# Performance work log

Measured on AMD Instinct MI355X. Metric: run time of the kernel, lower is better.

## Reference

```python
import jax, jax.numpy as jnp
import numpy as np

N = 10000
E = 160000
DIMS = [512, 512, 512, 256]  # in -> hidden -> hidden -> out (num_layers=3)
EPS = 1e-12  # F.normalize default eps


def _sage_layer(x, edge_index, Wl, b, Wr):
    # PyG SAGEConv (mean aggr, normalize=True):
    # out = lin_l(mean_{j in N(i)} x_j) + lin_r(x_i), then L2-normalize rows.
    src = edge_index[0]
    dst = edge_index[1]
    msg = x[src]  # [E, d] gather of source-node features
    agg = jax.ops.segment_sum(msg, dst, num_segments=N)  # [N, d]
    cnt = jax.ops.segment_sum(jnp.ones((E,), x.dtype), dst, num_segments=N)
    mean = agg / jnp.maximum(cnt, 1.0)[:, None]
    out = mean @ Wl.T + b + x @ Wr.T
    norm = jnp.sqrt(jnp.sum(out * out, axis=-1, keepdims=True))
    return out / jnp.maximum(norm, EPS)


def setup_inputs() -> dict:
    key = jax.random.key(0)
    ks = jax.random.split(key, 2 + 3 * len(DIMS))
    x = jax.random.normal(ks[0], (N, DIMS[0]), dtype=jnp.float32)
    edge_index = jax.random.randint(ks[1], (2, E), 0, N, dtype=jnp.int64)
    inp = {"x": x, "edge_index": edge_index}
    k = 2
    for i in range(len(DIMS) - 1):
        din, dout = DIMS[i], DIMS[i + 1]
        s = 1.0 / np.sqrt(din)
        inp[f"Wl{i}"] = jax.random.uniform(ks[k], (dout, din), jnp.float32, -s, s); k += 1
        inp[f"b{i}"] = jax.random.uniform(ks[k], (dout,), jnp.float32, -s, s); k += 1
        inp[f"Wr{i}"] = jax.random.uniform(ks[k], (dout, din), jnp.float32, -s, s); k += 1
    return inp


def reference(x, edge_index, Wl0, b0, Wr0, Wl1, b1, Wr1, Wl2, b2, Wr2):
    params = [(Wl0, b0, Wr0), (Wl1, b1, Wr1), (Wl2, b2, Wr2)]
    for Wl, b, Wr in params:
        x = _sage_layer(x, edge_index, Wl, b, Wr)
        x = jax.nn.relu(x)
        # F.dropout(training=False) is identity at inference
    return x
```

## Files before the change

kernel.cpp:

```cpp
#include <hip/hip_runtime.h>

#define NN 10000

typedef __attribute__((ext_vector_type(8))) short short8;
typedef __attribute__((ext_vector_type(4))) float f32x4;
typedef __attribute__((ext_vector_type(8))) _Float16 h16x8;
typedef __attribute__((ext_vector_type(4))) _Float16 h16x4;

__device__ __forceinline__ ushort f2b(float f) {
    union { float f; uint32_t u; } v; v.f = f;
    uint32_t u = v.u;
    return (ushort)((u + 0x7fffu + ((u >> 16) & 1u)) >> 16);
}
__device__ __forceinline__ uint packbf(float a, float b) {
    return (uint)f2b(a) | ((uint)f2b(b) << 16);
}
__device__ __forceinline__ float blo(uint u) {
    union { uint u; float f; } v; v.u = u << 16; return v.f;
}
__device__ __forceinline__ float bhi(uint u) {
    union { uint u; float f; } v; v.u = u & 0xffff0000u; return v.f;
}

__global__ __launch_bounds__(256) void count_dst(const int* __restrict__ dst,
                                                 int* __restrict__ counts, int E) {
    int i = blockIdx.x * 256 + threadIdx.x;
    if (i < E) atomicAdd(&counts[dst[i]], 1);
}

__global__ __launch_bounds__(256) void scan_local(const int* __restrict__ counts,
                                                  int* __restrict__ lpref,
                                                  int* __restrict__ bsum, int n) {
    __shared__ int tmp[256];
    int t = threadIdx.x, b = blockIdx.x;
    int i = b * 256 + t;
    int c = (i < n) ? counts[i] : 0;
    tmp[t] = c;
    __syncthreads();
    for (int off = 1; off < 256; off <<= 1) {
        int v = (t >= off) ? tmp[t - off] : 0;
        __syncthreads();
        tmp[t] += v;
        __syncthreads();
    }
    if (i < n) lpref[i] = tmp[t] - c;
    if (t == 255) bsum[b] = tmp[255];
}

__global__ __launch_bounds__(256) void scan_apply(const int* __restrict__ counts,
                                                  const int* __restrict__ lpref,
                                                  const int* __restrict__ bsum,
                                                  int* __restrict__ offsets,
                                                  int* __restrict__ cursor,
                                                  float* __restrict__ inv_cnt, int n) {
    __shared__ int sbase;
    int t = threadIdx.x, b = blockIdx.x;
    if (t == 0) {
        int s = 0;
        for (int j = 0; j < b; j++) s += bsum[j];
        sbase = s;
    }
    __syncthreads();
    int i = b * 256 + t;
    if (i < n) {
        int c = counts[i];
        int o = sbase + lpref[i];
        offsets[i] = o;
        cursor[i]  = o;
        inv_cnt[i] = 1.0f / fmaxf((float)c, 1.0f);
    }
}

__global__ __launch_bounds__(256) void scatter_edges(const int* __restrict__ src,
                                                     const int* __restrict__ dst,
                                                     int* __restrict__ cursor,
                                                     int* __restrict__ sorted_src, int E) {
    int i = blockIdx.x * 256 + threadIdx.x;
    if (i < E) {
        int p = atomicAdd(&cursor[dst[i]], 1);
        sorted_src[p] = src[i];
    }
}

__global__ __launch_bounds__(256) void cvt_all(const float* __restrict__ x,
                                               const float* __restrict__ Wl0,
                                               const float* __restrict__ Wr0,
                                               const float* __restrict__ Wl1,
                                               const float* __restrict__ Wr1,
                                               const float* __restrict__ Wl2,
                                               const float* __restrict__ Wr2,
                                               ushort* __restrict__ xbuf,
                                               ushort* __restrict__ Wc0,
                                               ushort* __restrict__ Wc1,
                                               ushort* __restrict__ Wc2,
                                               int* __restrict__ counts) {
    int i = blockIdx.x * 256 + threadIdx.x;
    const float* src;
    ushort* dst;
    if (i < 1280000) {
        int idx = i * 4;
        src = x + idx;
        dst = xbuf + idx;
    } else if (i < 1411072) {
        int j = (i - 1280000) * 4;
        int row = j >> 9, col = j & 511;
        src = (row < 512) ? (Wl0 + (size_t)row * 512 + col)
                          : (Wr0 + (size_t)(row - 512) * 512 + col);
        dst = Wc0 + j;
    } else if (i < 1542144) {
        int j = (i - 1411072) * 4;
        int row = j >> 9, col = j & 511;
        src = (row < 512) ? (Wl1 + (size_t)row * 512 + col)
                          : (Wr1 + (size_t)(row - 512) * 512 + col);
        dst = Wc1 + j;
    } else if (i < 1607680) {
        int j = (i - 1542144) * 4;
        int row = j >> 9, col = j & 511;
        src = (row < 256) ? (Wl2 + (size_t)row * 512 + col)
                          : (Wr2 + (size_t)(row - 256) * 512 + col);
        dst = Wc2 + j;
    } else if (i < 1610180) {
        int t = i - 1607680;
        int4 z = {0, 0, 0, 0};
        *(int4*)(counts + t * 4) = z;
        return;
    } else {
        return;
    }
    float4 v = *(const float4*)src;
    uint2 p;
    p.x = packbf(v.x, v.y);
    p.y = packbf(v.z, v.w);
    *(uint2*)dst = p;
}

__global__ __launch_bounds__(256) void gemm_split(const ushort* __restrict__ A,
                                                  const ushort* __restrict__ B,
                                                  ushort* __restrict__ G,
                                                  _Float16* __restrict__ R,
                                                  int M, int dout) {
    __shared__ ushort Asl[2][128 * 32];
    __shared__ ushort Bsl[2][128 * 32];
    const int tid  = threadIdx.x;
    const int w    = tid >> 6;
    const int lane = tid & 63;

    const int nbx = gridDim.x, nby = gridDim.y;
    const int nwg = nbx * nby;
    const int id  = blockIdx.y * nbx + blockIdx.x;
    const int qq  = nwg >> 3, rr = nwg & 7;
    const int xcd = id & 7, blk = id >> 3;
    const int swzid = (xcd < rr ? xcd * (qq + 1) : rr * (qq + 1) + (xcd - rr) * qq) + blk;
    const int bx = swzid % nbx, by = swzid / nbx;

    const int bm = by * 128, bn = bx * 128;
    const int wm = (w & 1) * 64, wn = (w >> 1) * 64;
    const int row16 = lane & 15, q = lane >> 4;

    f32x4 acc[4][4];
#pragma unroll
    for (int i = 0; i < 4; i++)
#pragma unroll
        for (int j = 0; j < 4; j++) acc[i][j] = (f32x4){0.f, 0.f, 0.f, 0.f};

    const int sc_r = lane >> 2;
    const int sc_s = lane & 3;
    const int koff = sc_s ^ ((sc_r >> 1) & 3);
    const int swz  = (row16 >> 1) & 3;

    auto stage = [&](int buf, int k0) {
#pragma unroll
        for (int c = 0; c < 2; c++) {
            int chunk = w * 2 + c;
            int rloc  = chunk * 16 + sc_r;
            int growA = bm + rloc; growA = growA < M ? growA : M - 1;
            const ushort* gpA = A + (size_t)growA * 512 + k0 + koff * 8;
            __builtin_amdgcn_global_load_lds(
                (const __attribute__((address_space(1))) uint32_t*)gpA,
                (__attribute__((address_space(3))) uint32_t*)&Asl[buf][chunk * 512],
                16, 0, 0);
            const ushort* gpB = B + (size_t)(bn + rloc) * 512 + k0 + koff * 8;
            __builtin_amdgcn_global_load_lds(
                (const __attribute__((address_space(1))) uint32_t*)gpB,
                (__attribute__((address_space(3))) uint32_t*)&Bsl[buf][chunk * 512],
                16, 0, 0);
        }
    };

    const int NT = 512 / 32;
    stage(0, 0);
    asm volatile("s_waitcnt vmcnt(0)" ::: "memory");
    __builtin_amdgcn_sched_barrier(0);
    __builtin_amdgcn_s_barrier();
    int cur = 0;

    for (int t = 0; t < NT; ++t) {
        const bool pref = (t + 1 < NT);
        if (pref) {
            stage(cur ^ 1, (t + 1) * 32);
            asm volatile("s_waitcnt vmcnt(4)" ::: "memory");
        } else {
            asm volatile("s_waitcnt vmcnt(0)" ::: "memory");
        }
        __builtin_amdgcn_sched_barrier(0);
        __builtin_amdgcn_s_barrier();

        short8 af[4], bfr[4];
        int s = q ^ swz;
#pragma unroll
        for (int i = 0; i < 4; i++) {
            int r = wm + i * 16 + row16;
            af[i] = *(const short8*)&Asl[cur][r * 32 + s * 8];
        }
#pragma unroll
        for (int j = 0; j < 4; j++) {
            int rn = wn + j * 16 + row16;
            bfr[j] = *(const short8*)&Bsl[cur][rn * 32 + s * 8];
        }
#pragma unroll
        for (int i = 0; i < 4; i++)
#pragma unroll
            for (int j = 0; j < 4; j++)
                acc[i][j] = __builtin_amdgcn_mfma_f32_16x16x32_bf16(
                    af[i], bfr[j], acc[i][j], 0, 0, 0);

        __builtin_amdgcn_sched_barrier(0);
        __builtin_amdgcn_s_barrier();
        cur ^= 1;
    }

    const bool isR = (bn >= dout);
#pragma unroll
    for (int i = 0; i < 4; i++) {
#pragma unroll
        for (int r2 = 0; r2 < 4; r2++) {
            int row = bm + wm + i * 16 + q * 4 + r2;
            if (row < M) {
                if (isR) {
                    _Float16* Rp = R + (size_t)row * dout + (bn - dout) + wn + row16;
#pragma unroll
                    for (int j = 0; j < 4; j++)
                        Rp[j * 16] = (_Float16)acc[i][j][r2];
                } else {
                    ushort* Gp = G + (size_t)row * dout + bn + wn + row16;
#pragma unroll
                    for (int j = 0; j < 4; j++)
                        Gp[j * 16] = f2b(acc[i][j][r2]);
                }
            }
        }
    }
}

template <int DOUT, bool FINAL>
__global__ __launch_bounds__(256) void aggfin(const ushort* __restrict__ G,
                                              const _Float16* __restrict__ R,
                                              const float* __restrict__ bias,
                                              const int* __restrict__ offsets,
                                              const int* __restrict__ counts,
                                              const int* __restrict__ sorted_src,
                                              const float* __restrict__ inv_cnt,
                                              ushort* __restrict__ xnext,
                                              float* __restrict__ outf, int n) {
    constexpr int PL = DOUT / 64;
    int wave = threadIdx.x >> 6;
    int lane = threadIdx.x & 63;
    int node = blockIdx.x * 4 + wave;
    if (node >= n) return;
    int start = offsets[node];
    int cnt   = counts[node];
    float inv = inv_cnt[node];

    float acc[PL];
#pragma unroll
    for (int k = 0; k < PL; k++) acc[k] = 0.f;

    if constexpr (DOUT == 512) {
        const uint* gp = (const uint*)G + lane * 4;
#define ACC8(v) do { \
        acc[0] += blo(v.x); acc[1] += bhi(v.x); \
        acc[2] += blo(v.y); acc[3] += bhi(v.y); \
        acc[4] += blo(v.z); acc[5] += bhi(v.z); \
        acc[6] += blo(v.w); acc[7] += bhi(v.w); } while (0)
        int e = 0;
        for (; e + 8 <= cnt; e += 8) {
            uint4 vv[8];
#pragma unroll
            for (int u = 0; u < 8; u++) {
                int s0 = sorted_src[start + e + u];
                vv[u] = *(const uint4*)(gp + (size_t)s0 * 256);
            }
#pragma unroll
            for (int u = 0; u < 8; u++) ACC8(vv[u]);
        }
        for (; e < cnt; e++) {
            int s0 = sorted_src[start + e];
            uint4 v0 = *(const uint4*)(gp + (size_t)s0 * 256);
            ACC8(v0);
        }
#undef ACC8
    } else {
        const uint* gp = (const uint*)G + lane * 2;
#define ACC4(v) do { \
        acc[0] += blo(v.x); acc[1] += bhi(v.x); \
        acc[2] += blo(v.y); acc[3] += bhi(v.y); } while (0)
        int e = 0;
        for (; e + 8 <= cnt; e += 8) {
            uint2 vv[8];
#pragma unroll
            for (int u = 0; u < 8; u++) {
                int s0 = sorted_src[start + e + u];
                vv[u] = *(const uint2*)(gp + (size_t)s0 * 128);
            }
#pragma unroll
            for (int u = 0; u < 8; u++) ACC4(vv[u]);
        }
        for (; e < cnt; e++) {
            int s0 = sorted_src[start + e];
            uint2 v0 = *(const uint2*)(gp + (size_t)s0 * 128);
            ACC4(v0);
        }
#undef ACC4
    }

    float v[PL];
    const _Float16* Rp = R + (size_t)node * DOUT + lane * PL;
    const float* Bp = bias + lane * PL;
    if constexpr (PL == 8) {
        h16x8 hv = *(const h16x8*)Rp;
#pragma unroll
        for (int k = 0; k < PL; k += 4) {
            float4 b4 = *(const float4*)(Bp + k);
            v[k + 0] = acc[k + 0] * inv + (float)hv[k + 0] + b4.x;
            v[k + 1] = acc[k + 1] * inv + (float)hv[k + 1] + b4.y;
            v[k + 2] = acc[k + 2] * inv + (float)hv[k + 2] + b4.z;
            v[k + 3] = acc[k + 3] * inv + (float)hv[k + 3] + b4.w;
        }
    } else {
        h16x4 hv = *(const h16x4*)Rp;
#pragma unroll
        for (int k = 0; k < PL; k += 4) {
            float4 b4 = *(const float4*)(Bp + k);
            v[k + 0] = acc[k + 0] * inv + (float)hv[k + 0] + b4.x;
            v[k + 1] = acc[k + 1] * inv + (float)hv[k + 1] + b4.y;
            v[k + 2] = acc[k + 2] * inv + (float)hv[k + 2] + b4.z;
            v[k + 3] = acc[k + 3] * inv + (float)hv[k + 3] + b4.w;
        }
    }

    float ss = 0.f;
#pragma unroll
    for (int k = 0; k < PL; k++) ss += v[k] * v[k];
#pragma unroll
    for (int m = 32; m >= 1; m >>= 1) ss += __shfl_xor(ss, m, 64);
    float scale = 1.0f / fmaxf(sqrtf(ss), 1e-12f);

    if constexpr (FINAL) {
        float* Op = outf + (size_t)node * DOUT + lane * PL;
#pragma unroll
        for (int k = 0; k < PL; k += 4) {
            float4 o;
            o.x = fmaxf(v[k + 0] * scale, 0.f);
            o.y = fmaxf(v[k + 1] * scale, 0.f);
            o.z = fmaxf(v[k + 2] * scale, 0.f);
            o.w = fmaxf(v[k + 3] * scale, 0.f);
            *(float4*)(Op + k) = o;
        }
    } else {
        uint4 o;
        float r0 = fmaxf(v[0] * scale, 0.f), r1 = fmaxf(v[1] * scale, 0.f);
        float r2 = fmaxf(v[2] * scale, 0.f), r3 = fmaxf(v[3] * scale, 0.f);
        float r4 = fmaxf(v[4] * scale, 0.f), r5 = fmaxf(v[5] * scale, 0.f);
        float r6 = fmaxf(v[6] * scale, 0.f), r7 = fmaxf(v[7] * scale, 0.f);
        o.x = packbf(r0, r1); o.y = packbf(r2, r3);
        o.z = packbf(r4, r5); o.w = packbf(r6, r7);
        *(uint4*)(xnext + (size_t)node * 512 + lane * 8) = o;
    }
}

extern "C" void kernel_launch(void* const* d_in, const int* in_sizes, int n_in,
                              void* d_out, int out_size, void* d_ws, size_t ws_size,
                              hipStream_t stream) {
    const float* x    = (const float*)d_in[0];
    const int*   edge = (const int*)d_in[1];
    const float* Wl0  = (const float*)d_in[2];
    const float* b0   = (const float*)d_in[3];
    const float* Wr0  = (const float*)d_in[4];
    const float* Wl1  = (const float*)d_in[5];
    const float* b1   = (const float*)d_in[6];
    const float* Wr1  = (const float*)d_in[7];
    const float* Wl2  = (const float*)d_in[8];
    const float* b2   = (const float*)d_in[9];
    const float* Wr2  = (const float*)d_in[10];

    const int E = in_sizes[1] / 2;

    char* ws = (char*)d_ws;
    int*      counts  = (int*)(ws + 0);
    int*      offsets = (int*)(ws + 40960);
    int*      cursor  = (int*)(ws + 81920);
    float*    invc    = (float*)(ws + 122880);
    int*      sorted  = (int*)(ws + 163840);
    ushort*   Wc0     = (ushort*)(ws + 819200);
    ushort*   Wc1     = (ushort*)(ws + 1867776);
    ushort*   Wc2     = (ushort*)(ws + 2916352);
    ushort*   xbuf    = (ushort*)(ws + 3440640);
    ushort*   Gbuf    = (ushort*)(ws + 13680640);
    _Float16* Rbuf    = (_Float16*)(ws + 23920640);
    int*      lpref   = (int*)(ws + 34160640);
    int*      bsum    = (int*)(ws + 34201600);

    cvt_all<<<(1610180 + 255) / 256, 256, 0, stream>>>(x, Wl0, Wr0, Wl1, Wr1, Wl2, Wr2,
                                                       xbuf, Wc0, Wc1, Wc2, counts);

    const int nsb = (NN + 255) / 256;
    count_dst<<<(E + 255) / 256, 256, 0, stream>>>(edge + E, counts, E);
    scan_local<<<nsb, 256, 0, stream>>>(counts, lpref, bsum, NN);
    scan_apply<<<nsb, 256, 0, stream>>>(counts, lpref, bsum, offsets, cursor, invc, NN);
    scatter_edges<<<(E + 255) / 256, 256, 0, stream>>>(edge, edge + E, cursor, sorted, E);

    const int gyM = (NN + 127) / 128;
    const int gb  = (NN + 3) / 4;

    gemm_split<<<dim3(8, gyM), 256, 0, stream>>>(xbuf, Wc0, Gbuf, Rbuf, NN, 512);
    aggfin<512, false><<<gb, 256, 0, stream>>>(Gbuf, Rbuf, b0, offsets, counts,
                                               sorted, invc, xbuf, nullptr, NN);
    gemm_split<<<dim3(8, gyM), 256, 0, stream>>>(xbuf, Wc1, Gbuf, Rbuf, NN, 512);
    aggfin<512, false><<<gb, 256, 0, stream>>>(Gbuf, Rbuf, b1, offsets, counts,
                                               sorted, invc, xbuf, nullptr, NN);
    gemm_split<<<dim3(4, gyM), 256, 0, stream>>>(xbuf, Wc2, Gbuf, Rbuf, NN, 256);
    aggfin<256, true><<<gb, 256, 0, stream>>>(Gbuf, Rbuf, b2, offsets, counts,
                                              sorted, invc, nullptr, (float*)d_out, NN);
}
```

Measured before the change: 233.9 us.

## Bucket CSR edges by source range to improve gather locality

The CSR build now counts edges per (destination, source-bucket) pair, using 16 buckets of 625 nodes each. It scans the 160k-entry count array and scatters edges so that each node's neighbor list is grouped by source range. The aim is more locality in the feature gathers inside aggfin, and a parallel reduction replaces the serial block-sum prefix in scan_apply. The cost is a larger scan (625 blocks instead of 40), an extra atomic per edge and more workspace. The hardcoded 625 divisor assumes N=10000.

```diff
diff --git a/kernel.cpp b/kernel.cpp
--- a/kernel.cpp
+++ b/kernel.cpp
@@ -1,6 +1,7 @@
 #include <hip/hip_runtime.h>
 
 #define NN 10000
+#define NBK 16
 
 typedef __attribute__((ext_vector_type(8))) short short8;
 typedef __attribute__((ext_vector_type(4))) float f32x4;
@@ -22,19 +23,25 @@
     union { uint u; float f; } v; v.u = u & 0xffff0000u; return v.f;
 }
 
-__global__ __launch_bounds__(256) void count_dst(const int* __restrict__ dst,
-                                                 int* __restrict__ counts, int E) {
+__global__ __launch_bounds__(256) void count_dst(const int* __restrict__ src,
+                                                 const int* __restrict__ dst,
+                                                 int* __restrict__ counts,
+                                                 int* __restrict__ counts2, int E) {
     int i = blockIdx.x * 256 + threadIdx.x;
-    if (i < E) atomicAdd(&counts[dst[i]], 1);
-}
-
-__global__ __launch_bounds__(256) void scan_local(const int* __restrict__ counts,
+    if (i < E) {
+        int d = dst[i], s = src[i];
+        atomicAdd(&counts[d], 1);
+        atomicAdd(&counts2[d * NBK + s / 625], 1);
+    }
+}
+
+__global__ __launch_bounds__(256) void scan_local(const int* __restrict__ counts2,
                                                   int* __restrict__ lpref,
                                                   int* __restrict__ bsum, int n) {
     __shared__ int tmp[256];
     int t = threadIdx.x, b = blockIdx.x;
     int i = b * 256 + t;
-    int c = (i < n) ? counts[i] : 0;
+    int c = (i < n) ? counts2[i] : 0;
     tmp[t] = c;
     __syncthreads();
     for (int off = 1; off < 256; off <<= 1) {
@@ -47,38 +54,44 @@
     if (t == 255) bsum[b] = tmp[255];
 }
 
-__global__ __launch_bounds__(256) void scan_apply(const int* __restrict__ counts,
-                                                  const int* __restrict__ lpref,
+__global__ __launch_bounds__(256) void scan_apply(const int* __restrict__ lpref,
                                                   const int* __restrict__ bsum,
-                                                  int* __restrict__ offsets,
-                                                  int* __restrict__ cursor,
+                                                  const int* __restrict__ counts,
+                                                  int* __restrict__ offsets2,
+                                                  int* __restrict__ cursor2,
                                                   float* __restrict__ inv_cnt, int n) {
-    __shared__ int sbase;
+    __shared__ int red[256];
     int t = threadIdx.x, b = blockIdx.x;
-    if (t == 0) {
-        int s = 0;
-        for (int j = 0; j < b; j++) s += bsum[j];
-        sbase = s;
-    }
+    int s = 0;
+    for (int j = t; j < b; j += 256) s += bsum[j];
+    red[t] = s;
     __syncthreads();
+    for (int off = 128; off >= 1; off >>= 1) {
+        if (t < off) red[t] += red[t + off];
+        __syncthreads();
+    }
+    int base = red[0];
     int i = b * 256 + t;
     if (i < n) {
-        int c = counts[i];
-        int o = sbase + lpref[i];
-        offsets[i] = o;
-        cursor[i]  = o;
-        inv_cnt[i] = 1.0f / fmaxf((float)c, 1.0f);
+        int o = base + lpref[i];
+        offsets2[i] = o;
+        cursor2[i]  = o;
+        if ((i & (NBK - 1)) == 0) {
+            int node = i / NBK;
+            inv_cnt[node] = 1.0f / fmaxf((float)counts[node], 1.0f);
+        }
     }
 }
 
 __global__ __launch_bounds__(256) void scatter_edges(const int* __restrict__ src,
                                                      const int* __restrict__ dst,
-                                                     int* __restrict__ cursor,
+                                                     int* __restrict__ cursor2,
                                                      int* __restrict__ sorted_src, int E) {
     int i = blockIdx.x * 256 + threadIdx.x;
     if (i < E) {
-        int p = atomicAdd(&cursor[dst[i]], 1);
-        sorted_src[p] = src[i];
+        int s = src[i], d = dst[i];
+        int p = atomicAdd(&cursor2[d * NBK + s / 625], 1);
+        sorted_src[p] = s;
     }
 }
 
@@ -93,7 +106,8 @@
                                                ushort* __restrict__ Wc0,
                                                ushort* __restrict__ Wc1,
                                                ushort* __restrict__ Wc2,
-                                               int* __restrict__ counts) {
+                                               int* __restrict__ counts,
+                                               int* __restrict__ counts2) {
     int i = blockIdx.x * 256 + threadIdx.x;
     const float* src;
     ushort* dst;
@@ -124,6 +138,11 @@
         int4 z = {0, 0, 0, 0};
         *(int4*)(counts + t * 4) = z;
         return;
+    } else if (i < 1650180) {
+        int t = i - 1610180;
+        int4 z = {0, 0, 0, 0};
+        *(int4*)(counts2 + t * 4) = z;
+        return;
     } else {
         return;
     }
@@ -256,7 +275,7 @@
 __global__ __launch_bounds__(256) void aggfin(const ushort* __restrict__ G,
                                               const _Float16* __restrict__ R,
                                               const float* __restrict__ bias,
-                                              const int* __restrict__ offsets,
+                                              const int* __restrict__ offsets2,
                                               const int* __restrict__ counts,
                                               const int* __restrict__ sorted_src,
                                               const float* __restrict__ inv_cnt,
@@ -267,7 +286,7 @@
     int lane = threadIdx.x & 63;
     int node = blockIdx.x * 4 + wave;
     if (node >= n) return;
-    int start = offsets[node];
+    int start = offsets2[node * NBK];
     int cnt   = counts[node];
     float inv = inv_cnt[node];
 
@@ -396,39 +415,41 @@
     const int E = in_sizes[1] / 2;
 
     char* ws = (char*)d_ws;
-    int*      counts  = (int*)(ws + 0);
-    int*      offsets = (int*)(ws + 40960);
-    int*      cursor  = (int*)(ws + 81920);
-    float*    invc    = (float*)(ws + 122880);
-    int*      sorted  = (int*)(ws + 163840);
-    ushort*   Wc0     = (ushort*)(ws + 819200);
-    ushort*   Wc1     = (ushort*)(ws + 1867776);
-    ushort*   Wc2     = (ushort*)(ws + 2916352);
-    ushort*   xbuf    = (ushort*)(ws + 3440640);
-    ushort*   Gbuf    = (ushort*)(ws + 13680640);
-    _Float16* Rbuf    = (_Float16*)(ws + 23920640);
-    int*      lpref   = (int*)(ws + 34160640);
-    int*      bsum    = (int*)(ws + 34201600);
-
-    cvt_all<<<(1610180 + 255) / 256, 256, 0, stream>>>(x, Wl0, Wr0, Wl1, Wr1, Wl2, Wr2,
-                                                       xbuf, Wc0, Wc1, Wc2, counts);
-
-    const int nsb = (NN + 255) / 256;
-    count_dst<<<(E + 255) / 256, 256, 0, stream>>>(edge + E, counts, E);
-    scan_local<<<nsb, 256, 0, stream>>>(counts, lpref, bsum, NN);
-    scan_apply<<<nsb, 256, 0, stream>>>(counts, lpref, bsum, offsets, cursor, invc, NN);
-    scatter_edges<<<(E + 255) / 256, 256, 0, stream>>>(edge, edge + E, cursor, sorted, E);
+    int*      counts   = (int*)(ws + 0);
+    float*    invc     = (float*)(ws + 40960);
+    int*      counts2  = (int*)(ws + 81920);
+    int*      lpref2   = (int*)(ws + 724992);
+    int*      offsets2 = (int*)(ws + 1368064);
+    int*      cursor2  = (int*)(ws + 2011136);
+    int*      bsum2    = (int*)(ws + 2654208);
+    int*      sorted   = (int*)(ws + 2658304);
+    ushort*   Wc0      = (ushort*)(ws + 3301376);
+    ushort*   Wc1      = (ushort*)(ws + 4349952);
+    ushort*   Wc2      = (ushort*)(ws + 5398528);
+    ushort*   xbuf     = (ushort*)(ws + 5922816);
+    ushort*   Gbuf     = (ushort*)(ws + 16162816);
+    _Float16* Rbuf     = (_Float16*)(ws + 26402816);
+
+    cvt_all<<<(1650180 + 255) / 256, 256, 0, stream>>>(x, Wl0, Wr0, Wl1, Wr1, Wl2, Wr2,
+                                                       xbuf, Wc0, Wc1, Wc2, counts, counts2);
+
+    const int NT2  = NN * NBK;
+    const int nsb2 = (NT2 + 255) / 256;
+    count_dst<<<(E + 255) / 256, 256, 0, stream>>>(edge, edge + E, counts, counts2, E);
+    scan_local<<<nsb2, 256, 0, stream>>>(counts2, lpref2, bsum2, NT2);
+    scan_apply<<<nsb2, 256, 0, stream>>>(lpref2, bsum2, counts, offsets2, cursor2, invc, NT2);
+    scatter_edges<<<(E + 255) / 256, 256, 0, stream>>>(edge, edge + E, cursor2, sorted, E);
 
     const int gyM = (NN + 127) / 128;
     const int gb  = (NN + 3) / 4;
 
     gemm_split<<<dim3(8, gyM), 256, 0, stream>>>(xbuf, Wc0, Gbuf, Rbuf, NN, 512);
-    aggfin<512, false><<<gb, 256, 0, stream>>>(Gbuf, Rbuf, b0, offsets, counts,
+    aggfin<512, false><<<gb, 256, 0, stream>>>(Gbuf, Rbuf, b0, offsets2, counts,
                                                sorted, invc, xbuf, nullptr, NN);
     gemm_split<<<dim3(8, gyM), 256, 0, stream>>>(xbuf, Wc1, Gbuf, Rbuf, NN, 512);
-    aggfin<512, false><<<gb, 256, 0, stream>>>(Gbuf, Rbuf, b1, offsets, counts,
+    aggfin<512, false><<<gb, 256, 0, stream>>>(Gbuf, Rbuf, b1, offsets2, counts,
                                                sorted, invc, xbuf, nullptr, NN);
     gemm_split<<<dim3(4, gyM), 256, 0, stream>>>(xbuf, Wc2, Gbuf, Rbuf, NN, 256);
-    aggfin<256, true><<<gb, 256, 0, stream>>>(Gbuf, Rbuf, b2, offsets, counts,
+    aggfin<256, true><<<gb, 256, 0, stream>>>(Gbuf, Rbuf, b2, offsets2, counts,
                                               sorted, invc, nullptr, (float*)d_out, NN);
 }
```

New measurement: 235.5 us. Within noise of the previous version (+0.7%).
